# Kernel optimization log

Hardware: AMD Instinct MI355X
Metric: run time of the kernel (lower is better)

The kernel has to match this reference:

```python
import jax, jax.numpy as jnp
import numpy as np

N = 100_000      # nodes
E = 1_600_000    # edges (avg degree 16)
D_IN = 128
D_OUT = 128
K = 64           # low-rank attention rank


def setup_inputs() -> dict:
    key = jax.random.key(0)
    ks = jax.random.split(key, 6)
    s = lambda d: 1.0 / np.sqrt(d)
    return {
        "x": jax.random.normal(ks[0], (N, D_IN), dtype=jnp.float32),
        "edge_index": jax.random.randint(ks[1], (2, E), 0, N, dtype=jnp.int32),
        "W_gcn": jax.random.normal(ks[2], (D_IN, D_OUT), dtype=jnp.float32) * s(D_IN),
        "b_gcn": jnp.zeros((D_OUT,), jnp.float32),
        "W_att": jax.random.normal(ks[3], (D_IN, 4 * K), dtype=jnp.float32) * s(D_IN),
        "b_att": jnp.zeros((4 * K,), jnp.float32),
        "W_red": jax.random.normal(ks[4], (D_OUT + 2 * K, D_OUT), dtype=jnp.float32) * s(D_OUT + 2 * K),
        "b_red": jnp.zeros((D_OUT,), jnp.float32),
    }


def _forward(x, W_gcn, b_gcn, W_att, b_att, W_red, b_red, edge_index):
    n = x.shape[0]
    # --- GCN conv (symmetric normalization, self-loops), dropout = identity (eval) ---
    loop = jnp.arange(n, dtype=edge_index.dtype)
    src = jnp.concatenate([edge_index[0], loop])
    dst = jnp.concatenate([edge_index[1], loop])
    deg = jax.ops.segment_sum(jnp.ones_like(dst, dtype=x.dtype), dst, num_segments=n)
    dinv = jax.lax.rsqrt(deg)                      # deg >= 1 due to self-loops
    norm = dinv[src] * dinv[dst]                   # [E+n]
    h = x @ W_gcn                                  # [n, D_OUT]
    agg = jax.ops.segment_sum(h[src] * norm[:, None], dst, num_segments=n) + b_gcn
    x_local = jax.nn.relu(agg)

    # --- Low-rank global attention (LRGA) ---
    t = jax.nn.relu(x @ W_att + b_att)             # [n, 4K]
    U, V, Z, T = jnp.split(t, 4, axis=1)           # each [n, K]
    # joint_normalize2: scalar 1/mean(U @ (V^T @ 1_n))
    D = 1.0 / jnp.mean(U @ (V.T @ jnp.ones((n, 1), x.dtype)))
    res = (U @ (V.T @ Z)) * D                      # [n, K]
    x_global = jnp.concatenate([res, T], axis=1)   # [n, 2K]

    # --- fuse + dim reduce ---
    return jnp.concatenate([x_local, x_global], axis=1) @ W_red + b_red


def reference(x, edge_index, W_gcn, b_gcn, W_att, b_att, W_red, b_red):
    return _forward(x, W_gcn, b_gcn, W_att, b_att, W_red, b_red, edge_index)
```

## Files before the change

### kernel.cpp

```cpp
#include <hip/hip_runtime.h>

#define DIN   128
#define DOUT  128
#define KR    64
#define TCOLS 256
#define WCOLS 384
#define P_RED 1024
#define PSTR  4224

typedef unsigned short ushort_t;
typedef __attribute__((ext_vector_type(8))) short bf16x8;
typedef __attribute__((ext_vector_type(4))) float f32x4;

__device__ __forceinline__ float bf2f(unsigned short u) {
  return __uint_as_float(((unsigned int)u) << 16);
}
__device__ __forceinline__ unsigned short f2bf(float f) {
  unsigned int b = __float_as_uint(f);
  b = b + 0x7FFFu + ((b >> 16) & 1u);
  return (unsigned short)(b >> 16);
}

__global__ __launch_bounds__(256) void k_init(int* __restrict__ degc, float* __restrict__ VtZ,
                                              float* __restrict__ colsum, int N) {
  int i = blockIdx.x * 256 + threadIdx.x;
  if (i < N) degc[i] = 1;
  if (i < 4096) VtZ[i] = 0.f;
  if (i < 128) colsum[i] = 0.f;
}

__global__ __launch_bounds__(256) void k_deg(const int* __restrict__ ei, int* __restrict__ degc, int E) {
  int e = blockIdx.x * 256 + threadIdx.x;
  if (e < E) atomicAdd(&degc[ei[E + e]], 1);
}

__global__ __launch_bounds__(256) void k_split(const float* __restrict__ x,
                                               ushort_t* __restrict__ xhF, ushort_t* __restrict__ xloF,
                                               int N, int total_slots) {
  int gid = blockIdx.x * 256 + threadIdx.x;
  int stride = gridDim.x * 256;
  for (; gid < total_slots; gid += stride) {
    int f = gid >> 6, l = gid & 63;
    int r16 = f >> 2, s = f & 3;
    int row = r16 * 16 + (l & 15);
    int k = s * 32 + ((l >> 4) << 3);
    ushort4 h0, h1, l0, l1;
    if (row < N) {
      float4 a = *(const float4*)&x[(size_t)row * DIN + k];
      float4 b = *(const float4*)&x[(size_t)row * DIN + k + 4];
      h0.x = f2bf(a.x); h0.y = f2bf(a.y); h0.z = f2bf(a.z); h0.w = f2bf(a.w);
      h1.x = f2bf(b.x); h1.y = f2bf(b.y); h1.z = f2bf(b.z); h1.w = f2bf(b.w);
      l0.x = f2bf(a.x - bf2f(h0.x)); l0.y = f2bf(a.y - bf2f(h0.y));
      l0.z = f2bf(a.z - bf2f(h0.z)); l0.w = f2bf(a.w - bf2f(h0.w));
      l1.x = f2bf(b.x - bf2f(h1.x)); l1.y = f2bf(b.y - bf2f(h1.y));
      l1.z = f2bf(b.z - bf2f(h1.z)); l1.w = f2bf(b.w - bf2f(h1.w));
    } else {
      h0 = make_ushort4(0, 0, 0, 0); h1 = h0; l0 = h0; l1 = h0;
    }
    ((ushort4*)xhF)[gid * 2] = h0;
    ((ushort4*)xhF)[gid * 2 + 1] = h1;
    ((ushort4*)xloF)[gid * 2] = l0;
    ((ushort4*)xloF)[gid * 2 + 1] = l1;
  }
}

__global__ __launch_bounds__(256) void k_wprep(const float* __restrict__ Wg, const float* __restrict__ Wa,
                                               ushort_t* __restrict__ whF, ushort_t* __restrict__ wlF) {
  int g = blockIdx.x * 256 + threadIdx.x;
  int f = g >> 6, l = g & 63;
  int c16 = f >> 2, s = f & 3;
  int col = c16 * 16 + (l & 15);
  int k = s * 32 + ((l >> 4) << 3);
#pragma unroll
  for (int j = 0; j < 8; ++j) {
    float v = (col < DOUT) ? Wg[(size_t)(k + j) * DOUT + col]
                           : Wa[(size_t)(k + j) * TCOLS + (col - DOUT)];
    ushort_t h = f2bf(v);
    whF[(size_t)g * 8 + j] = h;
    wlF[(size_t)g * 8 + j] = f2bf(v - bf2f(h));
  }
}

__global__ __launch_bounds__(256) void k_scan1(const int* __restrict__ degc, int* __restrict__ offs,
                                               int* __restrict__ bsums, int N) {
  __shared__ int s[256];
  int tid = threadIdx.x;
  int base = blockIdx.x * 1024 + tid * 4;
  int c[4], e[4];
#pragma unroll
  for (int q = 0; q < 4; ++q) c[q] = (base + q < N) ? (degc[base + q] - 1) : 0;
  e[0] = 0; e[1] = c[0]; e[2] = e[1] + c[1]; e[3] = e[2] + c[2];
  int tsum = e[3] + c[3];
  s[tid] = tsum; __syncthreads();
  for (int off = 1; off < 256; off <<= 1) {
    int v = (tid >= off) ? s[tid - off] : 0;
    __syncthreads();
    s[tid] += v;
    __syncthreads();
  }
  int tb = s[tid] - tsum;
#pragma unroll
  for (int q = 0; q < 4; ++q) if (base + q < N) offs[base + q] = tb + e[q];
  if (tid == 255) bsums[blockIdx.x] = s[255];
}

__global__ __launch_bounds__(128) void k_scan2(const int* __restrict__ bsums, int* __restrict__ boff,
                                               int* __restrict__ offs, int NBLK, int N) {
  __shared__ int s[128];
  int tid = threadIdx.x;
  int v = (tid < NBLK) ? bsums[tid] : 0;
  s[tid] = v; __syncthreads();
  for (int off = 1; off < 128; off <<= 1) {
    int u = (tid >= off) ? s[tid - off] : 0;
    __syncthreads();
    s[tid] += u;
    __syncthreads();
  }
  boff[tid] = s[tid] - v;
  if (tid == 127) offs[N] = s[127];
}

__global__ __launch_bounds__(256) void k_scan3(int* __restrict__ offs, const int* __restrict__ boff,
                                               const int* __restrict__ degc, float* __restrict__ dinv,
                                               int* __restrict__ cursor, int N) {
  int i = blockIdx.x * 256 + threadIdx.x;
  if (i < N) {
    offs[i] += boff[i >> 10];
    dinv[i] = rsqrtf((float)degc[i]);
    cursor[i] = 0;
  }
}

__global__ __launch_bounds__(256) void k_scatter(const int* __restrict__ ei, const int* __restrict__ offs,
                                                 int* __restrict__ cursor, const float* __restrict__ dinv,
                                                 int2* __restrict__ csr, int E) {
  int e = blockIdx.x * 256 + threadIdx.x;
  if (e < E) {
    int s = ei[e];
    int d = ei[E + e];
    int pos = atomicAdd(&cursor[d], 1);
    int2 q;
    q.x = s;
    q.y = __float_as_int(dinv[s] * dinv[d]);
    csr[offs[d] + pos] = q;
  }
}

#define LOADK(S, AH, AL, BH, BL)                                              \
  {                                                                           \
    _Pragma("unroll") for (int m_ = 0; m_ < 4; ++m_) {                        \
      size_t fo_ = (((size_t)(r16b + m_) * 4 + (S)) * 64 + lane) * 8;         \
      AH[m_] = *(const bf16x8*)&xhF[fo_];                                     \
      AL[m_] = *(const bf16x8*)&xloF[fo_];                                    \
    }                                                                         \
    _Pragma("unroll") for (int n_ = 0; n_ < 4; ++n_) {                        \
      size_t fo_ = (((size_t)(c16b + n_) * 4 + (S)) * 64 + lane) * 8;         \
      BH[n_] = *(const bf16x8*)&whF[fo_];                                     \
      BL[n_] = *(const bf16x8*)&wlF[fo_];                                     \
    }                                                                         \
  }

__global__ __launch_bounds__(256) void k_gemm1_mfma(const ushort_t* __restrict__ xhF,
                                                    const ushort_t* __restrict__ xloF,
                                                    const ushort_t* __restrict__ whF,
                                                    const ushort_t* __restrict__ wlF,
                                                    const float* __restrict__ ba,
                                                    ushort_t* __restrict__ hs, ushort_t* __restrict__ t,
                                                    int N, int ntiles) {
  int bid = blockIdx.x;
  int g = bid / 24;
  int rem = bid - g * 24;
  int colblk = rem >> 3;
  int ytile = g * 8 + (rem & 7);
  if (ytile >= ntiles) return;

  int tid = threadIdx.x;
  int lane = tid & 63;
  int wave = tid >> 6;
  int wr = wave >> 1, wc = wave & 1;
  int rowbase = ytile * 128 + wr * 64;
  int gcb = colblk * 128 + wc * 64;
  int r16b = ytile * 8 + wr * 4;
  int c16b = colblk * 8 + wc * 4;
  int lr = lane & 15;
  int rq = (lane >> 4) * 4;

  f32x4 acc[4][4] = {};
  bf16x8 ah[2][4], al[2][4], bh[2][4], bl[2][4];

  LOADK(0, ah[0], al[0], bh[0], bl[0]);
#pragma unroll
  for (int s = 0; s < 4; ++s) {
    int cur = s & 1, nxt = cur ^ 1;
    if (s < 3) LOADK(s + 1, ah[nxt], al[nxt], bh[nxt], bl[nxt]);
#pragma unroll
    for (int m = 0; m < 4; ++m)
#pragma unroll
      for (int n = 0; n < 4; ++n) {
        acc[m][n] = __builtin_amdgcn_mfma_f32_16x16x32_bf16(ah[cur][m], bl[cur][n], acc[m][n], 0, 0, 0);
        acc[m][n] = __builtin_amdgcn_mfma_f32_16x16x32_bf16(al[cur][m], bh[cur][n], acc[m][n], 0, 0, 0);
        acc[m][n] = __builtin_amdgcn_mfma_f32_16x16x32_bf16(ah[cur][m], bh[cur][n], acc[m][n], 0, 0, 0);
      }
  }

  if (colblk == 0) {
#pragma unroll
    for (int m = 0; m < 4; ++m)
#pragma unroll
      for (int i = 0; i < 4; ++i) {
        int row = rowbase + m * 16 + rq + i;
        if (row < N) {
#pragma unroll
          for (int n = 0; n < 4; ++n)
            hs[(size_t)row * DOUT + gcb + n * 16 + lr] = f2bf(acc[m][n][i]);
        }
      }
  } else {
    float bav[4];
#pragma unroll
    for (int n = 0; n < 4; ++n) bav[n] = ba[gcb - DOUT + n * 16 + lr];
#pragma unroll
    for (int m = 0; m < 4; ++m)
#pragma unroll
      for (int i = 0; i < 4; ++i) {
        int row = rowbase + m * 16 + rq + i;
        if (row < N) {
#pragma unroll
          for (int n = 0; n < 4; ++n)
            t[(size_t)row * TCOLS + gcb - DOUT + n * 16 + lr] =
                f2bf(fmaxf(acc[m][n][i] + bav[n], 0.f));
        }
      }
  }
}

__global__ __launch_bounds__(256) void k_red(const ushort_t* __restrict__ t, float* __restrict__ part,
                                             int N) {
  __shared__ float csh[512];
  int tid = threadIdx.x;
  int lane = tid & 63;
  int w = tid >> 6;
  int lr = lane & 15;
  int lk = (lane >> 4) * 8;
  int vcol = 64 + w * 16 + lr;
  int col2 = lane * 2;

  f32x4 acc[4] = {};
  float cs0 = 0.f, cs1 = 0.f;
  int ntiles = (N + 31) >> 5;

  for (int tile = blockIdx.x; tile < ntiles; tile += gridDim.x) {
    int r0 = tile * 32;
    const ushort_t* base = &t[(size_t)r0 * TCOLS];
    bf16x8 a, b[4];
    if (r0 + 32 <= N) {
#pragma unroll
      for (int j = 0; j < 8; ++j)
        ((short*)&a)[j] = (short)base[(size_t)(lk + j) * TCOLS + vcol];
#pragma unroll
      for (int n = 0; n < 4; ++n)
#pragma unroll
        for (int j = 0; j < 8; ++j)
          ((short*)&b[n])[j] = (short)base[(size_t)(lk + j) * TCOLS + 128 + n * 16 + lr];
#pragma unroll
      for (int j = 0; j < 8; ++j) {
        ushort2 u = *(const ushort2*)&base[(size_t)(w * 8 + j) * TCOLS + col2];
        cs0 += bf2f(u.x); cs1 += bf2f(u.y);
      }
    } else {
#pragma unroll
      for (int j = 0; j < 8; ++j) {
        int r = r0 + lk + j;
        ((short*)&a)[j] = (r < N) ? (short)t[(size_t)r * TCOLS + vcol] : (short)0;
      }
#pragma unroll
      for (int n = 0; n < 4; ++n)
#pragma unroll
        for (int j = 0; j < 8; ++j) {
          int r = r0 + lk + j;
          ((short*)&b[n])[j] = (r < N) ? (short)t[(size_t)r * TCOLS + 128 + n * 16 + lr] : (short)0;
        }
#pragma unroll
      for (int j = 0; j < 8; ++j) {
        int r = r0 + w * 8 + j;
        if (r < N) {
          ushort2 u = *(const ushort2*)&t[(size_t)r * TCOLS + col2];
          cs0 += bf2f(u.x); cs1 += bf2f(u.y);
        }
      }
    }
#pragma unroll
    for (int n = 0; n < 4; ++n)
      acc[n] = __builtin_amdgcn_mfma_f32_16x16x32_bf16(a, b[n], acc[n], 0, 0, 0);
  }

  float* pb = &part[(size_t)blockIdx.x * PSTR];
  int rq = (lane >> 4) * 4;
#pragma unroll
  for (int n = 0; n < 4; ++n)
#pragma unroll
    for (int i = 0; i < 4; ++i)
      pb[(w * 16 + rq + i) * 64 + n * 16 + lr] = acc[n][i];

  csh[tid] = cs0;
  csh[256 + tid] = cs1;
  __syncthreads();
  if (w == 0) {
    float t0 = csh[lane] + csh[64 + lane] + csh[128 + lane] + csh[192 + lane];
    float t1 = csh[256 + lane] + csh[320 + lane] + csh[384 + lane] + csh[448 + lane];
    pb[4096 + col2] = t0;
    pb[4096 + col2 + 1] = t1;
  }
}

__global__ __launch_bounds__(256) void k_redsum(const float* __restrict__ part,
                                                float* __restrict__ VtZ, float* __restrict__ colsum) {
  __shared__ float s[256];
  int tid = threadIdx.x;
  int j = blockIdx.x * 64 + (tid & 63);
  int bc = tid >> 6;
  float a = 0.f;
#pragma unroll 4
  for (int b = bc; b < P_RED; b += 4) a += part[(size_t)b * PSTR + j];
  s[tid] = a;
  __syncthreads();
  if (bc == 0) {
    float v = s[tid] + s[tid + 64] + s[tid + 128] + s[tid + 192];
    if (j < 4096) VtZ[j] = v;
    else colsum[j - 4096] = v;
  }
}

__global__ __launch_bounds__(64) void k_d(const float* __restrict__ colsum, float* __restrict__ Dws, int N) {
  __shared__ float s[64];
  int k = threadIdx.x;
  s[k] = colsum[k] * colsum[64 + k];
  __syncthreads();
  for (int off = 32; off > 0; off >>= 1) {
    if (k < off) s[k] += s[k + off];
    __syncthreads();
  }
  if (k == 0) {
    float p = s[0];
    Dws[0] = (p != 0.f) ? ((float)N / p) : 0.f;
  }
}

__global__ __launch_bounds__(256) void k_prep(const float* __restrict__ VtZ,
                                              const float* __restrict__ Dws,
                                              const float* __restrict__ Wr,
                                              ushort_t* __restrict__ weffT) {
  int c = blockIdx.x;
  int k = threadIdx.x;
  float v;
  if (k < 128 || k >= 192) {
    v = Wr[(size_t)k * DOUT + c];
  } else {
    float Dv = Dws[0];
    int kk = k - 128;
    float acc = 0.f;
#pragma unroll 8
    for (int j = 0; j < 64; ++j)
      acc += VtZ[kk * 64 + j] * Wr[(size_t)(128 + j) * DOUT + c];
    v = acc * Dv;
  }
  weffT[(size_t)c * 256 + k] = f2bf(v);
}

__global__ __launch_bounds__(256) void k_out_mfma(const ushort_t* __restrict__ xl,
                                                  const ushort_t* __restrict__ t,
                                                  const ushort_t* __restrict__ weffT,
                                                  const float* __restrict__ br,
                                                  float* __restrict__ out, int N) {
  int tid = threadIdx.x;
  int lane = tid & 63;
  int wave = tid >> 6;
  int wr = wave >> 1, wc = wave & 1;
  int rowbase = blockIdx.x * 128 + wr * 64;
  int cbase = wc * 64;
  int lr = lane & 15;
  int lk = (lane >> 4) * 8;

  int rows[4];
#pragma unroll
  for (int m = 0; m < 4; ++m) {
    int r = rowbase + m * 16 + lr;
    rows[m] = (r < N) ? r : (N - 1);
  }

  f32x4 acc[4][4] = {};

#pragma unroll
  for (int s = 0; s < 8; ++s) {
    int k0 = s * 32 + lk;
    bf16x8 a[4], b[4];
#pragma unroll
    for (int m = 0; m < 4; ++m) {
      const ushort_t* ap;
      if (s < 4)      ap = &xl[(size_t)rows[m] * DOUT + k0];
      else if (s < 6) ap = &t[(size_t)rows[m] * TCOLS + (k0 - 128)];
      else            ap = &t[(size_t)rows[m] * TCOLS + k0];
      a[m] = *(const bf16x8*)ap;
    }
#pragma unroll
    for (int n = 0; n < 4; ++n) {
      int c = cbase + n * 16 + lr;
      b[n] = *(const bf16x8*)&weffT[(size_t)c * 256 + k0];
    }
#pragma unroll
    for (int m = 0; m < 4; ++m)
#pragma unroll
      for (int n = 0; n < 4; ++n)
        acc[m][n] = __builtin_amdgcn_mfma_f32_16x16x32_bf16(a[m], b[n], acc[m][n], 0, 0, 0);
  }

  float brv[4];
#pragma unroll
  for (int n = 0; n < 4; ++n) brv[n] = br[cbase + n * 16 + lr];

  int rq = (lane >> 4) * 4;
#pragma unroll
  for (int m = 0; m < 4; ++m) {
#pragma unroll
    for (int i = 0; i < 4; ++i) {
      int row = rowbase + m * 16 + rq + i;
      if (row < N) {
#pragma unroll
        for (int n = 0; n < 4; ++n)
          out[(size_t)row * DOUT + cbase + n * 16 + lr] = acc[m][n][i] + brv[n];
      }
    }
  }
}

__global__ __launch_bounds__(256) void k_aggn(const ushort_t* __restrict__ hs, const int2* __restrict__ csr,
                                              const int* __restrict__ offs, const float* __restrict__ dinv,
                                              const float* __restrict__ bg,
                                              ushort_t* __restrict__ xl, int N) {
  int node = blockIdx.x * 4 + (threadIdx.x >> 6);
  int lane = threadIdx.x & 63;
  if (node >= N) return;
  int c2 = 2 * lane;
  float dn = dinv[node];
  ushort2 u = *(const ushort2*)&hs[(size_t)node * DOUT + c2];
  float a0 = dn * dn * bf2f(u.x);
  float a1 = dn * dn * bf2f(u.y);
  int e = offs[node], e1 = offs[node + 1];
  for (; e + 4 <= e1; e += 4) {
    int2 q0 = csr[e], q1 = csr[e + 1], q2 = csr[e + 2], q3 = csr[e + 3];
    ushort2 r0 = *(const ushort2*)&hs[(size_t)q0.x * DOUT + c2];
    ushort2 r1 = *(const ushort2*)&hs[(size_t)q1.x * DOUT + c2];
    ushort2 r2 = *(const ushort2*)&hs[(size_t)q2.x * DOUT + c2];
    ushort2 r3 = *(const ushort2*)&hs[(size_t)q3.x * DOUT + c2];
    float n0 = __int_as_float(q0.y), n1 = __int_as_float(q1.y);
    float n2 = __int_as_float(q2.y), n3 = __int_as_float(q3.y);
    a0 += n0 * bf2f(r0.x) + n1 * bf2f(r1.x) + n2 * bf2f(r2.x) + n3 * bf2f(r3.x);
    a1 += n0 * bf2f(r0.y) + n1 * bf2f(r1.y) + n2 * bf2f(r2.y) + n3 * bf2f(r3.y);
  }
  for (; e < e1; ++e) {
    int2 q = csr[e];
    ushort2 r = *(const ushort2*)&hs[(size_t)q.x * DOUT + c2];
    float n0 = __int_as_float(q.y);
    a0 += n0 * bf2f(r.x);
    a1 += n0 * bf2f(r.y);
  }
  ushort2 o;
  o.x = f2bf(fmaxf(a0 + bg[c2], 0.f));
  o.y = f2bf(fmaxf(a1 + bg[c2 + 1], 0.f));
  *(ushort2*)&xl[(size_t)node * DOUT + c2] = o;
}

extern "C" void kernel_launch(void* const* d_in, const int* in_sizes, int n_in,
                              void* d_out, int out_size, void* d_ws, size_t ws_size,
                              hipStream_t stream) {
  const float* x  = (const float*)d_in[0];
  const int* ei   = (const int*)d_in[1];
  const float* Wg = (const float*)d_in[2];
  const float* bg = (const float*)d_in[3];
  const float* Wa = (const float*)d_in[4];
  const float* ba = (const float*)d_in[5];
  const float* Wr = (const float*)d_in[6];
  const float* br = (const float*)d_in[7];
  float* out = (float*)d_out;

  const int N = in_sizes[0] / DIN;
  const int E = in_sizes[1] / 2;

  const int NT128 = (N + 127) / 128;
  const int N16P = NT128 * 8;
  const int NFRAG_A = N16P * 4;

  char* p = (char*)d_ws;
  auto alloc = [&](size_t bytes) {
    char* r = p;
    p += (bytes + 255) & ~(size_t)255;
    return r;
  };
  float* Dws    = (float*)alloc(256);
  float* colsum = (float*)alloc(128 * 4);
  float* VtZ    = (float*)alloc(4096 * 4);
  int*   bsums  = (int*)alloc(1024);
  int*   boff   = (int*)alloc(1024);
  ushort_t* weffT = (ushort_t*)alloc(128 * 256 * 2);
  ushort_t* whF = (ushort_t*)alloc((size_t)24 * 4 * 512 * 2);
  ushort_t* wlF = (ushort_t*)alloc((size_t)24 * 4 * 512 * 2);
  float* part   = (float*)alloc((size_t)P_RED * PSTR * 4);
  int*   degc   = (int*)alloc((size_t)N * 4);
  float* dinv   = (float*)alloc((size_t)N * 4);
  int*   offs   = (int*)alloc((size_t)(N + 1) * 4);
  int*   cursor = (int*)alloc((size_t)N * 4);
  int2*  csr    = (int2*)alloc((size_t)E * 8);
  ushort_t* xhF = (ushort_t*)alloc((size_t)NFRAG_A * 512 * 2);
  ushort_t* xloF= (ushort_t*)alloc((size_t)NFRAG_A * 512 * 2);
  ushort_t* hs  = (ushort_t*)alloc((size_t)N * DOUT * 2);
  ushort_t* t   = (ushort_t*)alloc((size_t)N * TCOLS * 2);
  ushort_t* xl  = (ushort_t*)alloc((size_t)N * DOUT * 2);
  (void)ws_size; (void)n_in; (void)out_size;

  const int GN = (N + 255) / 256;
  const int GE = (E + 255) / 256;
  const int NBLK = (N + 1023) / 1024;
  const int G1 = ((NT128 + 7) / 8) * 24;

  k_init<<<GN, 256, 0, stream>>>(degc, VtZ, colsum, N);
  k_deg<<<GE, 256, 0, stream>>>(ei, degc, E);
  k_split<<<2048, 256, 0, stream>>>(x, xhF, xloF, N, NFRAG_A * 64);
  k_wprep<<<24, 256, 0, stream>>>(Wg, Wa, whF, wlF);
  k_scan1<<<NBLK, 256, 0, stream>>>(degc, offs, bsums, N);
  k_scan2<<<1, 128, 0, stream>>>(bsums, boff, offs, NBLK, N);
  k_scan3<<<GN, 256, 0, stream>>>(offs, boff, degc, dinv, cursor, N);
  k_scatter<<<GE, 256, 0, stream>>>(ei, offs, cursor, dinv, csr, E);
  k_gemm1_mfma<<<G1, 256, 0, stream>>>(xhF, xloF, whF, wlF, ba, hs, t, N, NT128);
  k_red<<<P_RED, 256, 0, stream>>>(t, part, N);
  k_redsum<<<PSTR / 64, 256, 0, stream>>>(part, VtZ, colsum);
  k_d<<<1, 64, 0, stream>>>(colsum, Dws, N);
  k_prep<<<128, 256, 0, stream>>>(VtZ, Dws, Wr, weffT);
  k_aggn<<<(N + 3) / 4, 256, 0, stream>>>(hs, csr, offs, dinv, bg, xl, N);
  k_out_mfma<<<(N + 127) / 128, 256, 0, stream>>>(xl, t, weffT, br, out, N);
}
```

Baseline: 478.3 us.

## Replace random CSR scatter with two-pass bucketed scatter by destination range

Edges are first binned in shared memory by destination block of 1024 nodes and written contiguously into per-bucket buffers. A second kernel then scatters each bucket into the CSR, so the cursor atomics and CSR writes of one block stay within a small address range. The aim is to cut the cost of fully random global atomics and writes in the original scatter. In exchange it adds an extra kernel, an extra pass over the edge data through the bucket buffers, and an overflow fallback path.

```diff
diff --git a/kernel.cpp b/kernel.cpp
--- a/kernel.cpp
+++ b/kernel.cpp
@@ -22,11 +22,13 @@
 }
 
 __global__ __launch_bounds__(256) void k_init(int* __restrict__ degc, float* __restrict__ VtZ,
-                                              float* __restrict__ colsum, int N) {
+                                              float* __restrict__ colsum, int* __restrict__ bcur,
+                                              int N) {
   int i = blockIdx.x * 256 + threadIdx.x;
   if (i < N) degc[i] = 1;
   if (i < 4096) VtZ[i] = 0.f;
   if (i < 128) colsum[i] = 0.f;
+  if (i < 128) bcur[i] = 0;
 }
 
 __global__ __launch_bounds__(256) void k_deg(const int* __restrict__ ei, int* __restrict__ degc, int E) {
@@ -131,18 +133,86 @@
   }
 }
 
-__global__ __launch_bounds__(256) void k_scatter(const int* __restrict__ ei, const int* __restrict__ offs,
-                                                 int* __restrict__ cursor, const float* __restrict__ dinv,
-                                                 int2* __restrict__ csr, int E) {
-  int e = blockIdx.x * 256 + threadIdx.x;
-  if (e < E) {
-    int s = ei[e];
-    int d = ei[E + e];
-    int pos = atomicAdd(&cursor[d], 1);
-    int2 q;
-    q.x = s;
-    q.y = __float_as_int(dinv[s] * dinv[d]);
-    csr[offs[d] + pos] = q;
+__global__ __launch_bounds__(256) void k_bin(const int* __restrict__ ei, int* __restrict__ bcur,
+                                             int2* __restrict__ buckets, int* __restrict__ cursor,
+                                             const int* __restrict__ offs, const float* __restrict__ dinv,
+                                             int2* __restrict__ csr, int E, int B, int CAP) {
+  __shared__ int hist[128], pref[128], place[128], gbase[128];
+  __shared__ int2 st[4096];
+  int tid = threadIdx.x;
+  int e0 = blockIdx.x * 4096;
+  int nE = min(4096, E - e0);
+  if (nE <= 0) return;
+
+  if (tid < 128) { hist[tid] = 0; place[tid] = 0; }
+  __syncthreads();
+
+  int src[16], dst[16];
+#pragma unroll
+  for (int q = 0; q < 16; ++q) {
+    int idx = tid + q * 256;
+    if (idx < nE) {
+      src[q] = ei[e0 + idx];
+      dst[q] = ei[E + e0 + idx];
+      atomicAdd(&hist[dst[q] >> 10], 1);
+    }
+  }
+  __syncthreads();
+
+  if (tid < 128) pref[tid] = hist[tid];
+  __syncthreads();
+  for (int off = 1; off < 128; off <<= 1) {
+    int v = (tid < 128 && tid >= off) ? pref[tid - off] : 0;
+    __syncthreads();
+    if (tid < 128) pref[tid] += v;
+    __syncthreads();
+  }
+  if (tid < 128) pref[tid] -= hist[tid];
+  if (tid < B && hist[tid] > 0) gbase[tid] = atomicAdd(&bcur[tid], hist[tid]);
+  __syncthreads();
+
+#pragma unroll
+  for (int q = 0; q < 16; ++q) {
+    int idx = tid + q * 256;
+    if (idx < nE) {
+      int b = dst[q] >> 10;
+      int p = pref[b] + atomicAdd(&place[b], 1);
+      st[p] = make_int2(src[q], dst[q]);
+    }
+  }
+  __syncthreads();
+
+  for (int i = tid; i < nE; i += 256) {
+    int2 q = st[i];
+    int b = q.y >> 10;
+    int gp = gbase[b] + (i - pref[b]);
+    if (gp < CAP) {
+      buckets[(size_t)b * CAP + gp] = q;
+    } else {
+      int pos = atomicAdd(&cursor[q.y], 1);
+      int2 c;
+      c.x = q.x;
+      c.y = __float_as_int(dinv[q.x] * dinv[q.y]);
+      csr[offs[q.y] + pos] = c;
+    }
+  }
+}
+
+__global__ __launch_bounds__(256) void k_scatter2(const int2* __restrict__ buckets,
+                                                  const int* __restrict__ bcur,
+                                                  int* __restrict__ cursor, const int* __restrict__ offs,
+                                                  const float* __restrict__ dinv,
+                                                  int2* __restrict__ csr, int CAP) {
+  int b = blockIdx.x;
+  int n = min(bcur[b], CAP);
+  const int2* sp = &buckets[(size_t)b * CAP];
+  for (int i = threadIdx.x; i < n; i += 256) {
+    int2 q = sp[i];
+    int pos = atomicAdd(&cursor[q.y], 1);
+    int2 c;
+    c.x = q.x;
+    c.y = __float_as_int(dinv[q.x] * dinv[q.y]);
+    csr[offs[q.y] + pos] = c;
   }
 }
 
@@ -489,6 +559,8 @@
   const int NT128 = (N + 127) / 128;
   const int N16P = NT128 * 8;
   const int NFRAG_A = N16P * 4;
+  const int B = (N + 1023) >> 10;
+  const int CAP = ((E / (B > 0 ? B : 1)) * 3 / 2 + 255) & ~255;
 
   char* p = (char*)d_ws;
   auto alloc = [&](size_t bytes) {
@@ -501,6 +573,7 @@
   float* VtZ    = (float*)alloc(4096 * 4);
   int*   bsums  = (int*)alloc(1024);
   int*   boff   = (int*)alloc(1024);
+  int*   bcur   = (int*)alloc(1024);
   ushort_t* weffT = (ushort_t*)alloc(128 * 256 * 2);
   ushort_t* whF = (ushort_t*)alloc((size_t)24 * 4 * 512 * 2);
   ushort_t* wlF = (ushort_t*)alloc((size_t)24 * 4 * 512 * 2);
@@ -510,6 +583,7 @@
   int*   offs   = (int*)alloc((size_t)(N + 1) * 4);
   int*   cursor = (int*)alloc((size_t)N * 4);
   int2*  csr    = (int2*)alloc((size_t)E * 8);
+  int2*  buckets= (int2*)alloc((size_t)B * CAP * 8);
   ushort_t* xhF = (ushort_t*)alloc((size_t)NFRAG_A * 512 * 2);
   ushort_t* xloF= (ushort_t*)alloc((size_t)NFRAG_A * 512 * 2);
   ushort_t* hs  = (ushort_t*)alloc((size_t)N * DOUT * 2);
@@ -521,15 +595,17 @@
   const int GE = (E + 255) / 256;
   const int NBLK = (N + 1023) / 1024;
   const int G1 = ((NT128 + 7) / 8) * 24;
-
-  k_init<<<GN, 256, 0, stream>>>(degc, VtZ, colsum, N);
+  const int GBIN = (E + 4095) / 4096;
+
+  k_init<<<GN, 256, 0, stream>>>(degc, VtZ, colsum, bcur, N);
   k_deg<<<GE, 256, 0, stream>>>(ei, degc, E);
   k_split<<<2048, 256, 0, stream>>>(x, xhF, xloF, N, NFRAG_A * 64);
   k_wprep<<<24, 256, 0, stream>>>(Wg, Wa, whF, wlF);
   k_scan1<<<NBLK, 256, 0, stream>>>(degc, offs, bsums, N);
   k_scan2<<<1, 128, 0, stream>>>(bsums, boff, offs, NBLK, N);
   k_scan3<<<GN, 256, 0, stream>>>(offs, boff, degc, dinv, cursor, N);
-  k_scatter<<<GE, 256, 0, stream>>>(ei, offs, cursor, dinv, csr, E);
+  k_bin<<<GBIN, 256, 0, stream>>>(ei, bcur, buckets, cursor, offs, dinv, csr, E, B, CAP);
+  k_scatter2<<<B, 256, 0, stream>>>(buckets, bcur, cursor, offs, dinv, csr, CAP);
   k_gemm1_mfma<<<G1, 256, 0, stream>>>(xhF, xloF, whF, wlF, ba, hs, t, N, NT128);
   k_red<<<P_RED, 256, 0, stream>>>(t, part, N);
   k_redsum<<<PSTR / 64, 256, 0, stream>>>(part, VtZ, colsum);
```

Result: no change. 487.6 us (+2.0%).
